# Kernel tuning notes

Measured on AMD Instinct MI355X. Metric: run time of the kernel, lower is better.

Reference implementation:

```python
import jax, jax.numpy as jnp
import numpy as np

EPS = 1e-12  # torch F.normalize eps
SIGMA_RBF = 1.0  # rbf bandwidth (init arg sigma=1)


def _l2norm(v, axis=-1):
    return v / jnp.maximum(jnp.linalg.norm(v, axis=axis, keepdims=True), EPS)


def setup_inputs() -> dict:
    key = jax.random.key(0)
    kx, kw, kb, ku, kc = jax.random.split(key, 5)
    B, C, E, F = 512, 100, 2048, 128
    x = jax.random.normal(kx, (B, E), dtype=jnp.float32)
    # per-class Linear weights [C, F, E] and biases [C, F] (torch Linear layout: out x in)
    bound = 1.0 / np.sqrt(E)
    W = jax.random.uniform(kw, (C, F, E), minval=-bound, maxval=bound, dtype=jnp.float32)
    b = jax.random.uniform(kb, (C, F), minval=-bound, maxval=bound, dtype=jnp.float32)
    # spectral-norm power-iteration vectors u (one per class, normalized)
    u = _l2norm(jax.random.normal(ku, (C, F), dtype=jnp.float32))
    # centroid buffer c (EMA means; randn stand-in for a trained state)
    c = jax.random.normal(kc, (C, F), dtype=jnp.float32)
    return {"x": x, "W": W, "b": b, "u": u, "c": c}


def reference(x, W, b, u, c):
    # --- spectral norm: one power-iteration step per class (torch default) ---
    v = _l2norm(jnp.einsum('cfe,cf->ce', W, u))        # v = normalize(W^T u)  [C,E]
    u2 = _l2norm(jnp.einsum('cfe,ce->cf', W, v))       # u = normalize(W v)    [C,F]
    sigma = jnp.einsum('cf,cfe,ce->c', u2, W, v)       # sigma = u^T W v       [C]
    Wn = W / sigma[:, None, None]
    # --- fused per-class linear projections: z[b,c,f] ---
    z = jnp.einsum('be,cfe->bcf', x, Wn) + b[None, :, :]
    # --- RBF to centroids: exp(-||c - z||^2 / (2 sigma^2)) ---
    dist2 = jnp.sum((c[None, :, :] - z) ** 2, axis=-1)  # [B, C]
    probs = jnp.exp(-dist2 / (2.0 * SIGMA_RBF ** 2))
    return probs
```

## Files before the change

kernel.cpp:

```cpp
#include <hip/hip_runtime.h>
#include <math.h>

#define B_ 512
#define C_ 100
#define E_ 2048
#define F_ 128

typedef _Float16 f16x8 __attribute__((ext_vector_type(8)));
typedef float    f32x4 __attribute__((ext_vector_type(4)));

#define AS1q __attribute__((address_space(1)))
#define AS3q __attribute__((address_space(3)))

__device__ __forceinline__ void gl_lds16(const void* g, void* lds_base) {
    __builtin_amdgcn_global_load_lds((const AS1q void*)g, (AS3q void*)lds_base, 16, 0, 0);
}

__global__ __launch_bounds__(256)
void k_conv(const float* __restrict__ W, _Float16* __restrict__ Wh,
            const float* __restrict__ x, _Float16* __restrict__ xh) {
    const int blk = blockIdx.x;
    const float* src; _Float16* dst; size_t base;
    if (blk < 800) { src = W; dst = Wh; base = (size_t)blk * 32768 + threadIdx.x * 8; }
    else           { src = x; dst = xh; base = (size_t)(blk - 800) * 32768 + threadIdx.x * 8; }
#pragma unroll
    for (int it = 0; it < 16; ++it) {
        const size_t idx = base + (size_t)it * 2048;
        float4 a = *(const float4*)(src + idx);
        float4 b = *(const float4*)(src + idx + 4);
        f16x8 h;
        h[0] = (_Float16)a.x; h[1] = (_Float16)a.y; h[2] = (_Float16)a.z; h[3] = (_Float16)a.w;
        h[4] = (_Float16)b.x; h[5] = (_Float16)b.y; h[6] = (_Float16)b.z; h[7] = (_Float16)b.w;
        *(f16x8*)(dst + idx) = h;
    }
}

__global__ __launch_bounds__(256, 2)
void k_gram_y(const _Float16* __restrict__ Wh, const float* __restrict__ u,
              float* __restrict__ y) {
    const int chunk = blockIdx.x;
    const int c  = blockIdx.y;
    const int t  = threadIdx.x;
    const int w  = t >> 6;
    const int l  = t & 63;
    const int wm = w & 1, wn = w >> 1;
    const int ln = l & 15, quad = l >> 4;

    __shared__ _Float16 Ts[128 * 64];

    f32x4 acc[4][4];
#pragma unroll
    for (int mt = 0; mt < 4; ++mt)
#pragma unroll
        for (int nt = 0; nt < 4; ++nt) acc[mt][nt] = (f32x4){0.f, 0.f, 0.f, 0.f};

    const int lr = l >> 3;
    const int lg = (l & 7) ^ lr;
    const _Float16* wsrc = Wh + ((size_t)c * F_ + w * 32 + lr) * E_ + lg * 8;
    const int kbase = chunk * 256;

    for (int k0 = kbase; k0 < kbase + 256; k0 += 64) {
#pragma unroll
        for (int q = 0; q < 4; ++q)
            gl_lds16(wsrc + (size_t)q * 8 * E_ + k0, &Ts[(w * 4 + q) * 512]);
        __syncthreads();

#pragma unroll
        for (int kk = 0; kk < 64; kk += 32) {
            const int g0 = (kk >> 3) + quad;
            const int sw = (g0 ^ (ln & 7)) * 8;
            f16x8 av[4], bv[4];
#pragma unroll
            for (int mt = 0; mt < 4; ++mt)
                av[mt] = *(const f16x8*)&Ts[(wm * 64 + mt * 16 + ln) * 64 + sw];
#pragma unroll
            for (int nt = 0; nt < 4; ++nt)
                bv[nt] = *(const f16x8*)&Ts[(wn * 64 + nt * 16 + ln) * 64 + sw];
#pragma unroll
            for (int mt = 0; mt < 4; ++mt)
#pragma unroll
                for (int nt = 0; nt < 4; ++nt)
                    acc[mt][nt] = __builtin_amdgcn_mfma_f32_16x16x32_f16(
                        av[mt], bv[nt], acc[mt][nt], 0, 0, 0);
        }
        __syncthreads();
    }

    const float* uc = u + (size_t)c * F_;
    float un[4];
#pragma unroll
    for (int nt = 0; nt < 4; ++nt) un[nt] = uc[wn * 64 + nt * 16 + ln];

#pragma unroll
    for (int mt = 0; mt < 4; ++mt) {
#pragma unroll
        for (int r = 0; r < 4; ++r) {
            float py = acc[mt][0][r] * un[0];
            py = fmaf(acc[mt][1][r], un[1], py);
            py = fmaf(acc[mt][2][r], un[2], py);
            py = fmaf(acc[mt][3][r], un[3], py);
            py += __shfl_xor(py, 1, 64);
            py += __shfl_xor(py, 2, 64);
            py += __shfl_xor(py, 4, 64);
            py += __shfl_xor(py, 8, 64);
            if (ln == 0) {
                int m = wm * 64 + mt * 16 + quad * 4 + r;
                atomicAdd(&y[(size_t)c * F_ + m], py);
            }
        }
    }
}

__global__ __launch_bounds__(64)
void k_rsig(const float* __restrict__ u, const float* __restrict__ y,
            float* __restrict__ rsig) {
    const int c = blockIdx.x;
    const int l = threadIdx.x;
    float y0 = y[(size_t)c * F_ + l],      y1 = y[(size_t)c * F_ + 64 + l];
    float u0 = u[(size_t)c * F_ + l],      u1 = u[(size_t)c * F_ + 64 + l];
    float nv = u0 * y0 + u1 * y1;
    float ts = y0 * y0 + y1 * y1;
    for (int off = 32; off; off >>= 1) {
        nv += __shfl_down(nv, off, 64);
        ts += __shfl_down(ts, off, 64);
    }
    if (l == 0) rsig[c] = sqrtf(nv / ts);
}

__global__ __launch_bounds__(256, 2)
void k_main(const _Float16* __restrict__ xh, const _Float16* __restrict__ Wh,
            const float* __restrict__ bias, const float* __restrict__ cent,
            const float* __restrict__ rsig, float* __restrict__ out) {
    const int c  = blockIdx.y;
    const int b0 = blockIdx.x * 128;
    const int t  = threadIdx.x;
    const int w  = t >> 6;
    const int l  = t & 63;
    const int wm = w & 1, wn = w >> 1;
    const int ln = l & 15, quad = l >> 4;

    __shared__ _Float16 Xs[128 * 64];
    __shared__ _Float16 Ws[128 * 64];

    f32x4 acc[4][4];
#pragma unroll
    for (int mt = 0; mt < 4; ++mt)
#pragma unroll
        for (int nt = 0; nt < 4; ++nt) acc[mt][nt] = (f32x4){0.f, 0.f, 0.f, 0.f};

    const int lr = l >> 3;
    const int lg = (l & 7) ^ lr;
    const _Float16* xsrc = xh + (size_t)(b0 + w * 32 + lr) * E_ + lg * 8;
    const _Float16* wsrc = Wh + ((size_t)c * F_ + w * 32 + lr) * E_ + lg * 8;

    for (int k0 = 0; k0 < E_; k0 += 64) {
#pragma unroll
        for (int q = 0; q < 4; ++q)
            gl_lds16(xsrc + (size_t)q * 8 * E_ + k0, &Xs[(w * 4 + q) * 512]);
#pragma unroll
        for (int q = 0; q < 4; ++q)
            gl_lds16(wsrc + (size_t)q * 8 * E_ + k0, &Ws[(w * 4 + q) * 512]);
        __syncthreads();

#pragma unroll
        for (int kk = 0; kk < 64; kk += 32) {
            const int g0 = (kk >> 3) + quad;
            const int sw = (g0 ^ (ln & 7)) * 8;
            f16x8 av[4], bv[4];
#pragma unroll
            for (int mt = 0; mt < 4; ++mt)
                av[mt] = *(const f16x8*)&Xs[(wm * 64 + mt * 16 + ln) * 64 + sw];
#pragma unroll
            for (int nt = 0; nt < 4; ++nt)
                bv[nt] = *(const f16x8*)&Ws[(wn * 64 + nt * 16 + ln) * 64 + sw];
#pragma unroll
            for (int mt = 0; mt < 4; ++mt)
#pragma unroll
                for (int nt = 0; nt < 4; ++nt)
                    acc[mt][nt] = __builtin_amdgcn_mfma_f32_16x16x32_f16(
                        av[mt], bv[nt], acc[mt][nt], 0, 0, 0);
        }
        __syncthreads();
    }

    const float rsigma = rsig[c];

    float bi[4], ce[4];
#pragma unroll
    for (int nt = 0; nt < 4; ++nt) {
        int f = wn * 64 + nt * 16 + ln;
        bi[nt] = bias[c * F_ + f];
        ce[nt] = cent[c * F_ + f];
    }

    float* red = (float*)&Xs[0];

#pragma unroll
    for (int mt = 0; mt < 4; ++mt) {
#pragma unroll
        for (int r = 0; r < 4; ++r) {
            float part = 0.f;
#pragma unroll
            for (int nt = 0; nt < 4; ++nt) {
                float z = fmaf(acc[mt][nt][r], rsigma, bi[nt]);
                float d = ce[nt] - z;
                part = fmaf(d, d, part);
            }
            part += __shfl_xor(part, 1, 64);
            part += __shfl_xor(part, 2, 64);
            part += __shfl_xor(part, 4, 64);
            part += __shfl_xor(part, 8, 64);
            if (ln == 0) {
                int m = wm * 64 + mt * 16 + quad * 4 + r;
                red[m * 2 + wn] = part;
            }
        }
    }
    __syncthreads();
    if (t < 128) {
        float d2 = red[t * 2] + red[t * 2 + 1];
        out[(size_t)(b0 + t) * C_ + c] = expf(-0.5f * d2);
    }
}

extern "C" void kernel_launch(void* const* d_in, const int* in_sizes, int n_in,
                              void* d_out, int out_size, void* d_ws, size_t ws_size,
                              hipStream_t stream) {
    const float* x  = (const float*)d_in[0];
    const float* W  = (const float*)d_in[1];
    const float* b  = (const float*)d_in[2];
    const float* u  = (const float*)d_in[3];
    const float* cc = (const float*)d_in[4];
    float* out = (float*)d_out;

    char* ws = (char*)d_ws;
    _Float16* Wh   = (_Float16*)ws;
    _Float16* xh   = (_Float16*)(ws + (size_t)C_ * F_ * E_ * 2);
    float*    yv   = (float*)(ws + (size_t)C_ * F_ * E_ * 2 + (size_t)B_ * E_ * 2);
    float*    rsig = yv + (size_t)C_ * F_;

    hipMemsetAsync(yv, 0, (size_t)C_ * F_ * sizeof(float), stream);

    k_conv<<<832, 256, 0, stream>>>(W, Wh, x, xh);

    dim3 ggrid(8, C_);
    k_gram_y<<<ggrid, 256, 0, stream>>>(Wh, u, yv);
    k_rsig<<<C_, 64, 0, stream>>>(u, yv, rsig);

    dim3 grid(B_ / 128, C_);
    k_main<<<grid, 256, 0, stream>>>(xh, Wh, b, cc, rsig, out);
}
```

Before: 232.0 us.

## Fuse fp16 conversion into Gram kernel and fold sigma reduction into main kernel

The fp32-to-fp16 conversion of W now happens inside the Gram kernel: each block converts its own chunk, writes it to global memory for the main kernel and stores it straight into LDS. The x conversion runs in extra blocks of the same launch. Per-chunk partial y vectors go to a buffer instead of being added atomically, and k_main reduces them and computes 1/sigma at its start. This removes the memset, the k_rsig launch, the separate conversion pass over W and the atomics, but each of the 400 k_main blocks now redoes the small sigma reduction. The Gram kernel's loads also become synchronous register loads rather than async global-to-LDS transfers.

```diff
diff --git a/kernel.cpp b/kernel.cpp
--- a/kernel.cpp
+++ b/kernel.cpp
@@ -16,31 +16,30 @@
     __builtin_amdgcn_global_load_lds((const AS1q void*)g, (AS3q void*)lds_base, 16, 0, 0);
 }
 
-__global__ __launch_bounds__(256)
-void k_conv(const float* __restrict__ W, _Float16* __restrict__ Wh,
-            const float* __restrict__ x, _Float16* __restrict__ xh) {
-    const int blk = blockIdx.x;
-    const float* src; _Float16* dst; size_t base;
-    if (blk < 800) { src = W; dst = Wh; base = (size_t)blk * 32768 + threadIdx.x * 8; }
-    else           { src = x; dst = xh; base = (size_t)(blk - 800) * 32768 + threadIdx.x * 8; }
-#pragma unroll
-    for (int it = 0; it < 16; ++it) {
-        const size_t idx = base + (size_t)it * 2048;
-        float4 a = *(const float4*)(src + idx);
-        float4 b = *(const float4*)(src + idx + 4);
-        f16x8 h;
-        h[0] = (_Float16)a.x; h[1] = (_Float16)a.y; h[2] = (_Float16)a.z; h[3] = (_Float16)a.w;
-        h[4] = (_Float16)b.x; h[5] = (_Float16)b.y; h[6] = (_Float16)b.z; h[7] = (_Float16)b.w;
-        *(f16x8*)(dst + idx) = h;
-    }
-}
-
 __global__ __launch_bounds__(256, 2)
-void k_gram_y(const _Float16* __restrict__ Wh, const float* __restrict__ u,
-              float* __restrict__ y) {
-    const int chunk = blockIdx.x;
-    const int c  = blockIdx.y;
-    const int t  = threadIdx.x;
+void k_gram(const float* __restrict__ W, _Float16* __restrict__ Wh,
+            const float* __restrict__ x, _Float16* __restrict__ xh,
+            const float* __restrict__ u, float* __restrict__ ychunks) {
+    const int b = blockIdx.x;
+    const int t = threadIdx.x;
+
+    if (b >= 800) {
+        const size_t base = (size_t)(b - 800) * 32768 + t * 8;
+#pragma unroll
+        for (int it = 0; it < 16; ++it) {
+            const size_t idx = base + (size_t)it * 2048;
+            float4 a  = *(const float4*)(x + idx);
+            float4 bb = *(const float4*)(x + idx + 4);
+            f16x8 h;
+            h[0] = (_Float16)a.x;  h[1] = (_Float16)a.y;  h[2] = (_Float16)a.z;  h[3] = (_Float16)a.w;
+            h[4] = (_Float16)bb.x; h[5] = (_Float16)bb.y; h[6] = (_Float16)bb.z; h[7] = (_Float16)bb.w;
+            *(f16x8*)(xh + idx) = h;
+        }
+        return;
+    }
+
+    const int c     = b >> 3;
+    const int chunk = b & 7;
     const int w  = t >> 6;
     const int l  = t & 63;
     const int wm = w & 1, wn = w >> 1;
@@ -54,15 +53,33 @@
 #pragma unroll
         for (int nt = 0; nt < 4; ++nt) acc[mt][nt] = (f32x4){0.f, 0.f, 0.f, 0.f};
 
-    const int lr = l >> 3;
-    const int lg = (l & 7) ^ lr;
-    const _Float16* wsrc = Wh + ((size_t)c * F_ + w * 32 + lr) * E_ + lg * 8;
+    const int r  = t >> 1;
+    const int cb = (t & 1) * 32;
+    const float* wsrc = W  + ((size_t)c * F_ + r) * E_ + cb;
+    _Float16*    wdst = Wh + ((size_t)c * F_ + r) * E_ + cb;
     const int kbase = chunk * 256;
 
     for (int k0 = kbase; k0 < kbase + 256; k0 += 64) {
-#pragma unroll
-        for (int q = 0; q < 4; ++q)
-            gl_lds16(wsrc + (size_t)q * 8 * E_ + k0, &Ts[(w * 4 + q) * 512]);
+        float4 f[8];
+#pragma unroll
+        for (int j = 0; j < 8; ++j) f[j] = *(const float4*)(wsrc + k0 + j * 4);
+        f16x8 h[4];
+#pragma unroll
+        for (int j = 0; j < 4; ++j) {
+            h[j][0] = (_Float16)f[2*j].x;   h[j][1] = (_Float16)f[2*j].y;
+            h[j][2] = (_Float16)f[2*j].z;   h[j][3] = (_Float16)f[2*j].w;
+            h[j][4] = (_Float16)f[2*j+1].x; h[j][5] = (_Float16)f[2*j+1].y;
+            h[j][6] = (_Float16)f[2*j+1].z; h[j][7] = (_Float16)f[2*j+1].w;
+        }
+#pragma unroll
+        for (int j = 0; j < 4; ++j) *(f16x8*)(wdst + k0 + j * 8) = h[j];
+
+        __syncthreads();
+#pragma unroll
+        for (int j = 0; j < 4; ++j) {
+            const int g = (cb >> 3) + j;
+            *(f16x8*)&Ts[r * 64 + ((g ^ (r & 7)) << 3)] = h[j];
+        }
         __syncthreads();
 
 #pragma unroll
@@ -83,7 +100,6 @@
                     acc[mt][nt] = __builtin_amdgcn_mfma_f32_16x16x32_f16(
                         av[mt], bv[nt], acc[mt][nt], 0, 0, 0);
         }
-        __syncthreads();
     }
 
     const float* uc = u + (size_t)c * F_;
@@ -91,46 +107,39 @@
 #pragma unroll
     for (int nt = 0; nt < 4; ++nt) un[nt] = uc[wn * 64 + nt * 16 + ln];
 
+    __syncthreads();
+    float* red = (float*)&Ts[0];
+
 #pragma unroll
     for (int mt = 0; mt < 4; ++mt) {
 #pragma unroll
-        for (int r = 0; r < 4; ++r) {
-            float py = acc[mt][0][r] * un[0];
-            py = fmaf(acc[mt][1][r], un[1], py);
-            py = fmaf(acc[mt][2][r], un[2], py);
-            py = fmaf(acc[mt][3][r], un[3], py);
+        for (int rr = 0; rr < 4; ++rr) {
+            float py = acc[mt][0][rr] * un[0];
+            py = fmaf(acc[mt][1][rr], un[1], py);
+            py = fmaf(acc[mt][2][rr], un[2], py);
+            py = fmaf(acc[mt][3][rr], un[3], py);
             py += __shfl_xor(py, 1, 64);
             py += __shfl_xor(py, 2, 64);
             py += __shfl_xor(py, 4, 64);
             py += __shfl_xor(py, 8, 64);
             if (ln == 0) {
-                int m = wm * 64 + mt * 16 + quad * 4 + r;
-                atomicAdd(&y[(size_t)c * F_ + m], py);
+                int m = wm * 64 + mt * 16 + quad * 4 + rr;
+                red[m * 2 + wn] = py;
             }
         }
     }
-}
-
-__global__ __launch_bounds__(64)
-void k_rsig(const float* __restrict__ u, const float* __restrict__ y,
-            float* __restrict__ rsig) {
-    const int c = blockIdx.x;
-    const int l = threadIdx.x;
-    float y0 = y[(size_t)c * F_ + l],      y1 = y[(size_t)c * F_ + 64 + l];
-    float u0 = u[(size_t)c * F_ + l],      u1 = u[(size_t)c * F_ + 64 + l];
-    float nv = u0 * y0 + u1 * y1;
-    float ts = y0 * y0 + y1 * y1;
-    for (int off = 32; off; off >>= 1) {
-        nv += __shfl_down(nv, off, 64);
-        ts += __shfl_down(ts, off, 64);
-    }
-    if (l == 0) rsig[c] = sqrtf(nv / ts);
+    __syncthreads();
+    if (t < 128) {
+        float yv = red[t * 2] + red[t * 2 + 1];
+        ychunks[((size_t)chunk * C_ + c) * F_ + t] = yv;
+    }
 }
 
 __global__ __launch_bounds__(256, 2)
 void k_main(const _Float16* __restrict__ xh, const _Float16* __restrict__ Wh,
             const float* __restrict__ bias, const float* __restrict__ cent,
-            const float* __restrict__ rsig, float* __restrict__ out) {
+            const float* __restrict__ u, const float* __restrict__ ychunks,
+            float* __restrict__ out) {
     const int c  = blockIdx.y;
     const int b0 = blockIdx.x * 128;
     const int t  = threadIdx.x;
@@ -141,6 +150,24 @@
 
     __shared__ _Float16 Xs[128 * 64];
     __shared__ _Float16 Ws[128 * 64];
+    __shared__ float red2[2][2];
+    __shared__ float s_rsig;
+
+    if (t < 128) {
+        float yf = 0.f;
+#pragma unroll
+        for (int ch = 0; ch < 8; ++ch)
+            yf += ychunks[((size_t)ch * C_ + c) * F_ + t];
+        float nvp = u[(size_t)c * F_ + t] * yf;
+        float tsp = yf * yf;
+        for (int off = 32; off; off >>= 1) {
+            nvp += __shfl_down(nvp, off, 64);
+            tsp += __shfl_down(tsp, off, 64);
+        }
+        if (l == 0) { red2[w][0] = nvp; red2[w][1] = tsp; }
+    }
+    __syncthreads();
+    if (t == 0) s_rsig = sqrtf((red2[0][0] + red2[1][0]) / (red2[0][1] + red2[1][1]));
 
     f32x4 acc[4][4];
 #pragma unroll
@@ -183,7 +210,7 @@
         __syncthreads();
     }
 
-    const float rsigma = rsig[c];
+    const float rsigma = s_rsig;
 
     float bi[4], ce[4];
 #pragma unroll
@@ -234,19 +261,12 @@
     float* out = (float*)d_out;
 
     char* ws = (char*)d_ws;
-    _Float16* Wh   = (_Float16*)ws;
-    _Float16* xh   = (_Float16*)(ws + (size_t)C_ * F_ * E_ * 2);
-    float*    yv   = (float*)(ws + (size_t)C_ * F_ * E_ * 2 + (size_t)B_ * E_ * 2);
-    float*    rsig = yv + (size_t)C_ * F_;
-
-    hipMemsetAsync(yv, 0, (size_t)C_ * F_ * sizeof(float), stream);
-
-    k_conv<<<832, 256, 0, stream>>>(W, Wh, x, xh);
-
-    dim3 ggrid(8, C_);
-    k_gram_y<<<ggrid, 256, 0, stream>>>(Wh, u, yv);
-    k_rsig<<<C_, 64, 0, stream>>>(u, yv, rsig);
+    _Float16* Wh      = (_Float16*)ws;
+    _Float16* xh      = (_Float16*)(ws + (size_t)C_ * F_ * E_ * 2);
+    float*    ychunks = (float*)(ws + (size_t)C_ * F_ * E_ * 2 + (size_t)B_ * E_ * 2);
+
+    k_gram<<<832, 256, 0, stream>>>(W, Wh, x, xh, u, ychunks);
 
     dim3 grid(B_ / 128, C_);
-    k_main<<<grid, 256, 0, stream>>>(xh, Wh, b, cc, rsig, out);
-}
+    k_main<<<grid, 256, 0, stream>>>(xh, Wh, b, cc, u, ychunks, out);
+}
```

Measured after the change: 221.8 us. 1.05x faster.
